# Kernel tuning notes

Hardware: AMD Instinct MI355X
Metric: run time of the kernel (lower is better)

The kernel has to match this reference:

```python
import jax, jax.numpy as jnp
import numpy as np

D_MODEL = 1024
NUM_HEADS = 16
HEAD_DIM = D_MODEL // NUM_HEADS
SCALE = HEAD_DIM ** -0.5
LN_EPS = 1e-5
Q_EPS = 1e-5


def bit_quant(W):
    # BitNet b1.58 ternary weight quantization with straight-through estimator.
    gamma = jnp.mean(jnp.abs(W))
    Wq = jnp.clip(jnp.round(W / (gamma + Q_EPS)), -1.0, 1.0) * gamma
    return W + jax.lax.stop_gradient(Wq - W)


def layer_norm(x, gamma, beta):
    mu = jnp.mean(x, axis=-1, keepdims=True)
    var = jnp.mean(jnp.square(x - mu), axis=-1, keepdims=True)
    return (x - mu) * jax.lax.rsqrt(var + LN_EPS) * gamma + beta


def setup_inputs() -> dict:
    key = jax.random.key(0)
    ks = jax.random.split(key, 8)
    B, T, T_ctx, C = 4, 1024, 2048, D_MODEL
    w_std = C ** -0.5
    return {
        "x": jax.random.normal(ks[0], (B, T, C), jnp.float32),
        "context": jax.random.normal(ks[1], (B, T_ctx, C), jnp.float32),
        "Wq": jax.random.normal(ks[2], (C, C), jnp.float32) * w_std,
        "bq": jnp.zeros((C,), jnp.float32),
        "Wk": jax.random.normal(ks[3], (C, C), jnp.float32) * w_std,
        "bk": jnp.zeros((C,), jnp.float32),
        "Wv": jax.random.normal(ks[4], (C, C), jnp.float32) * w_std,
        "bv": jnp.zeros((C,), jnp.float32),
        "Wo": jax.random.normal(ks[5], (C, C), jnp.float32) * w_std,
        "bo": jnp.zeros((C,), jnp.float32),
        "ln_gamma": jnp.ones((C,), jnp.float32),
        "ln_beta": jnp.zeros((C,), jnp.float32),
    }


def reference(x, context, Wq, bq, Wk, bk, Wv, bv, Wo, bo, ln_gamma, ln_beta):
    B, T, C = x.shape
    T_ctx = context.shape[1]
    residual = x
    xn = layer_norm(x, ln_gamma, ln_beta)
    # BitNet-quantized projections (torch Linear: y = x @ W.T + b)
    q = xn @ bit_quant(Wq).T + bq                      # [B,T,C]
    k = context @ bit_quant(Wk).T + bk                 # [B,T_ctx,C]
    v = context @ bit_quant(Wv).T + bv                 # [B,T_ctx,C]
    q = q.reshape(B, T, NUM_HEADS, HEAD_DIM)
    k = k.reshape(B, T_ctx, NUM_HEADS, HEAD_DIM)
    v = v.reshape(B, T_ctx, NUM_HEADS, HEAD_DIM)
    scores = jnp.einsum("bqhd,bkhd->bhqk", q, k) * SCALE   # [B,H,T,T_ctx]
    probs = jax.nn.softmax(scores, axis=-1)
    out = jnp.einsum("bhqk,bkhd->bqhd", probs, v).reshape(B, T, C)
    return residual + (out @ bit_quant(Wo).T + bo)
```

## Files before the change

### kernel.cpp

```cpp
#include <hip/hip_runtime.h>
#include <hip/hip_bf16.h>

typedef __attribute__((ext_vector_type(8))) short s8x;
typedef __attribute__((ext_vector_type(4))) float f4x;
typedef unsigned short u16;
typedef unsigned int u32;

#define T_ 1024
#define TC_ 2048
#define SCLOG2E 0.1803368801111243f

__device__ __forceinline__ u16 f2bf(float f) {
    u32 u = __float_as_uint(f);
    return (u16)((u + 0x7fffu + ((u >> 16) & 1u)) >> 16);
}

#if defined(__has_builtin)
#if __has_builtin(__builtin_amdgcn_cvt_pk_bf16_f32)
#define HAVE_PK 1
#endif
#endif

__device__ __forceinline__ u32 pack2bf(float a, float b) {
#ifdef HAVE_PK
    typedef __attribute__((ext_vector_type(2))) __bf16 bf2t;
    bf2t r = __builtin_amdgcn_cvt_pk_bf16_f32(a, b);
    u32 u;
    __builtin_memcpy(&u, &r, 4);
    return u;
#else
    return (u32)f2bf(a) | ((u32)f2bf(b) << 16);
#endif
}

__device__ __forceinline__ void gload16(const void* g, void* l) {
    __builtin_amdgcn_global_load_lds((const __attribute__((address_space(1))) u32*)g,
                                     (__attribute__((address_space(3))) u32*)l, 16, 0, 0);
}

__global__ __launch_bounds__(256) void absmean_k(const float* __restrict__ W0, const float* __restrict__ W1,
                                                 const float* __restrict__ W2, const float* __restrict__ W3,
                                                 float* __restrict__ gsum) {
    int wi = blockIdx.y;
    const float* W = (wi == 0) ? W0 : (wi == 1) ? W1 : (wi == 2) ? W2 : W3;
    const int n4 = (1024 * 1024) / 4;
    float s = 0.f;
    int stride = gridDim.x * blockDim.x;
    for (int i = blockIdx.x * blockDim.x + threadIdx.x; i < n4; i += stride) {
        float4 v = ((const float4*)W)[i];
        s += fabsf(v.x) + fabsf(v.y) + fabsf(v.z) + fabsf(v.w);
    }
#pragma unroll
    for (int off = 32; off; off >>= 1) s += __shfl_down(s, off, 64);
    __shared__ float ps[4];
    if ((threadIdx.x & 63) == 0) ps[threadIdx.x >> 6] = s;
    __syncthreads();
    if (threadIdx.x == 0) atomicAdd(gsum + wi, ps[0] + ps[1] + ps[2] + ps[3]);
}

__global__ __launch_bounds__(256) void prep_k(
        const float* __restrict__ x, const float* __restrict__ lng, const float* __restrict__ lnb,
        u16* __restrict__ xn,
        const float* __restrict__ ctx, u16* __restrict__ ctxb,
        const float* __restrict__ W0, const float* __restrict__ W1,
        const float* __restrict__ W2, const float* __restrict__ W3,
        u16* __restrict__ D0, u16* __restrict__ D1, u16* __restrict__ D2, u16* __restrict__ D3,
        const float* __restrict__ gsum) {
    __shared__ float ps[8];
    int bx = blockIdx.x, t = threadIdx.x;
    if (bx < 4096) {
        int row = bx;
        float4 xv = ((const float4*)(x + (long)row * 1024))[t];
        float s = xv.x + xv.y + xv.z + xv.w;
        float s2 = xv.x * xv.x + xv.y * xv.y + xv.z * xv.z + xv.w * xv.w;
#pragma unroll
        for (int off = 32; off; off >>= 1) { s += __shfl_down(s, off, 64); s2 += __shfl_down(s2, off, 64); }
        if ((t & 63) == 0) { ps[t >> 6] = s; ps[4 + (t >> 6)] = s2; }
        __syncthreads();
        float S = ps[0] + ps[1] + ps[2] + ps[3];
        float S2 = ps[4] + ps[5] + ps[6] + ps[7];
        float mu = S * (1.f / 1024.f);
        float var = S2 * (1.f / 1024.f) - mu * mu;
        float rstd = rsqrtf(var + 1e-5f);
        float4 gv = ((const float4*)lng)[t];
        float4 bv = ((const float4*)lnb)[t];
        uint2 o;
        o.x = pack2bf((xv.x - mu) * rstd * gv.x + bv.x, (xv.y - mu) * rstd * gv.y + bv.y);
        o.y = pack2bf((xv.z - mu) * rstd * gv.z + bv.z, (xv.w - mu) * rstd * gv.w + bv.w);
        ((uint2*)(xn + (long)row * 1024))[t] = o;
    } else if (bx < 12288) {
        int i = (bx - 4096) * 256 + t;
        float4 v = ((const float4*)ctx)[i];
        uint2 o = {pack2bf(v.x, v.y), pack2bf(v.z, v.w)};
        ((uint2*)ctxb)[i] = o;
    } else {
        int wi = (bx - 12288) >> 10;
        const float* W = (wi == 0) ? W0 : (wi == 1) ? W1 : (wi == 2) ? W2 : W3;
        u16* D = (wi == 0) ? D0 : (wi == 1) ? D1 : (wi == 2) ? D2 : D3;
        float inv = 1.0f / (gsum[wi] * (1.0f / 1048576.0f) + 1e-5f);
        int i = ((bx - 12288) & 1023) * 256 + t;
        float4 wv = ((const float4*)W)[i];
        uint2 o;
        o.x = pack2bf(fminf(1.f, fmaxf(-1.f, rintf(wv.x * inv))),
                      fminf(1.f, fmaxf(-1.f, rintf(wv.y * inv))));
        o.y = pack2bf(fminf(1.f, fmaxf(-1.f, rintf(wv.z * inv))),
                      fminf(1.f, fmaxf(-1.f, rintf(wv.w * inv))));
        ((uint2*)D)[i] = o;
    }
}

__global__ __launch_bounds__(256) void gemm_fused(
        const u16* __restrict__ xn, const u16* __restrict__ ctxb,
        const u16* __restrict__ wtq, const u16* __restrict__ wtk, const u16* __restrict__ wtv,
        const float* __restrict__ bq, const float* __restrict__ bk, const float* __restrict__ bv,
        const float* __restrict__ gsum,
        u16* __restrict__ qb, u16* __restrict__ kb, u16* __restrict__ vtb) {
    __shared__ __align__(16) char smem[32768];
    int tid = threadIdx.x;
    int w = tid >> 6, l = tid & 63, lq = l & 15, lh = l >> 4;
    int wm = (w >> 1) * 64, wn = (w & 1) * 64;
    int bx = blockIdx.x;
    int xcd = bx & 7;
    int prob, m0, n0, gidx;
    const u16 *A, *Wt;
    const float* bias;
    float sc;
    if (bx < 256) {
        int local = bx >> 3;
        prob = 0; A = xn; Wt = wtq; bias = bq; sc = SCLOG2E; gidx = 0;
        m0 = (xcd * 4 + (local & 3)) * 128;
        n0 = (local >> 2) * 128;
    } else {
        int b = bx - 256;
        int local3 = b >> 3;
        int kv = local3 & 1;
        int idx = local3 >> 1;
        prob = 1 + kv; A = ctxb;
        Wt = kv ? wtv : wtk; bias = kv ? bv : bk; sc = 1.0f; gidx = 1 + kv;
        m0 = (xcd * 8 + (idx & 7)) * 128;
        n0 = (idx >> 3) * 128;
    }
    char* AsB = smem;
    char* BsB = smem + 16384;
    f4x acc[4][4] = {};
    int rb = tid >> 3;
    int cg = (tid & 7) ^ (rb & 7);
    const u16* Ag = A + (long)m0 * 1024 + cg * 8;
    const u16* Bg = Wt + (long)n0 * 1024 + cg * 8;
    for (int k0 = 0; k0 < 1024; k0 += 64) {
        __syncthreads();
#pragma unroll
        for (int i = 0; i < 4; i++) {
            gload16(Ag + (long)(i * 32 + rb) * 1024 + k0, AsB + (i * 256 + tid) * 16);
            gload16(Bg + (long)(i * 32 + rb) * 1024 + k0, BsB + (i * 256 + tid) * 16);
        }
        __syncthreads();
#pragma unroll
        for (int s = 0; s < 2; s++) {
            int sl = (s * 4 + lh) ^ (lq & 7);
            s8x af[4], bfr[4];
#pragma unroll
            for (int i = 0; i < 4; i++) {
                af[i] = *(const s8x*)(AsB + (wm + i * 16 + lq) * 128 + sl * 16);
                bfr[i] = *(const s8x*)(BsB + (wn + i * 16 + lq) * 128 + sl * 16);
            }
#pragma unroll
            for (int i = 0; i < 4; i++)
#pragma unroll
                for (int j = 0; j < 4; j++)
                    acc[i][j] = __builtin_amdgcn_mfma_f32_16x16x32_bf16(af[i], bfr[j], acc[i][j], 0, 0, 0);
        }
    }
    float gamma = gsum[gidx] * (1.0f / 1048576.0f) * sc;
    if (prob < 2) {
        u16* outq = (prob == 0) ? qb : kb;
        int tshift = (prob == 0) ? 10 : 11;
        int tmask = (1 << tshift) - 1;
#pragma unroll
        for (int i = 0; i < 4; i++) {
            int gr = m0 + wm + i * 16 + lh * 4;
#pragma unroll
            for (int j = 0; j < 4; j++) {
                int gc = n0 + wn + j * 16 + lq;
                float bb = bias[gc] * sc;
                int h = gc >> 6, d = gc & 63;
#pragma unroll
                for (int r = 0; r < 4; r++) {
                    int row = gr + r;
                    int bidx = row >> tshift, tt = row & tmask;
                    outq[((((long)(bidx * 16 + h)) << tshift) + tt) * 64 + d] = f2bf(acc[i][j][r] * gamma + bb);
                }
            }
        }
    } else {
        __syncthreads();
        char* Ct = smem;
#pragma unroll
        for (int i = 0; i < 4; i++) {
            int tt = wm + i * 16 + lh * 4;
#pragma unroll
            for (int j = 0; j < 4; j++) {
                int c = wn + j * 16 + lq;
                float bb = bias[n0 + c];
                uint2 pk;
                pk.x = pack2bf(acc[i][j][0] * gamma + bb, acc[i][j][1] * gamma + bb);
                pk.y = pack2bf(acc[i][j][2] * gamma + bb, acc[i][j][3] * gamma + bb);
                int slot = (tt >> 3) ^ (c & 15);
                *(uint2*)(Ct + c * 256 + slot * 16 + (tt & 7) * 2) = pk;
            }
        }
        __syncthreads();
        int bb2 = m0 >> 11, t0 = m0 & 2047;
#pragma unroll
        for (int it = 0; it < 8; it++) {
            int e = it * 256 + tid;
            int c = e >> 4, ch = e & 15;
            int slot = ch ^ (c & 15);
            s8x v = *(const s8x*)(Ct + c * 256 + slot * 16);
            int gcg = n0 + c;
            int h = gcg >> 6, d = gcg & 63;
            *(s8x*)(vtb + ((long)((bb2 * 16 + h) * 64 + d)) * TC_ + t0 + ch * 8) = v;
        }
    }
}

__global__ __launch_bounds__(256) void gemm_o(const u16* __restrict__ A, const u16* __restrict__ Wt,
                                              const float* __restrict__ bias, const float* __restrict__ gsum,
                                              const float* __restrict__ residual, float* __restrict__ outr) {
    __shared__ __align__(16) char smem[24576];
    int tid = threadIdx.x;
    int w = tid >> 6, l = tid & 63, lq = l & 15, lh = l >> 4;
    int wm = (w >> 1) * 64, wn = (w & 1) * 32;
    int bx = blockIdx.x;
    int xcd = bx & 7, local = bx >> 3;
    int m0 = (xcd * 4 + (local & 3)) * 128;
    int n0 = (local >> 2) * 64;
    char* AsB = smem;
    char* BsB = smem + 16384;
    f4x acc[4][2] = {};
    int rb = tid >> 3;
    int cg = (tid & 7) ^ (rb & 7);
    const u16* Ag = A + (long)m0 * 1024 + cg * 8;
    const u16* Bg = Wt + (long)n0 * 1024 + cg * 8;
    for (int k0 = 0; k0 < 1024; k0 += 64) {
        __syncthreads();
#pragma unroll
        for (int i = 0; i < 4; i++)
            gload16(Ag + (long)(i * 32 + rb) * 1024 + k0, AsB + (i * 256 + tid) * 16);
#pragma unroll
        for (int i = 0; i < 2; i++)
            gload16(Bg + (long)(i * 32 + rb) * 1024 + k0, BsB + (i * 256 + tid) * 16);
        __syncthreads();
#pragma unroll
        for (int s = 0; s < 2; s++) {
            int sl = (s * 4 + lh) ^ (lq & 7);
            s8x af[4], bfr[2];
#pragma unroll
            for (int i = 0; i < 4; i++)
                af[i] = *(const s8x*)(AsB + (wm + i * 16 + lq) * 128 + sl * 16);
#pragma unroll
            for (int j = 0; j < 2; j++)
                bfr[j] = *(const s8x*)(BsB + (wn + j * 16 + lq) * 128 + sl * 16);
#pragma unroll
            for (int i = 0; i < 4; i++)
#pragma unroll
                for (int j = 0; j < 2; j++)
                    acc[i][j] = __builtin_amdgcn_mfma_f32_16x16x32_bf16(af[i], bfr[j], acc[i][j], 0, 0, 0);
        }
    }
    float gamma = gsum[3] * (1.0f / 1048576.0f);
#pragma unroll
    for (int i = 0; i < 4; i++) {
        int gr = m0 + wm + i * 16 + lh * 4;
#pragma unroll
        for (int j = 0; j < 2; j++) {
            int gc = n0 + wn + j * 16 + lq;
            float bb = bias[gc];
#pragma unroll
            for (int r = 0; r < 4; r++) {
                long idx = (long)(gr + r) * 1024 + gc;
                outr[idx] = residual[idx] + acc[i][j][r] * gamma + bb;
            }
        }
    }
}

__global__ __launch_bounds__(512) void attn_k(const u16* __restrict__ qh, const u16* __restrict__ kh,
                                              const u16* __restrict__ vth, u16* __restrict__ attn) {
    __shared__ __align__(16) char smem[51200];
    int tid = threadIdx.x, w = tid >> 6, l = tid & 63, lq = l & 15, lh = l >> 4;
    int bh = blockIdx.x, q0 = blockIdx.y * 128;
    const u16* qp = qh + ((long)bh * T_ + q0) * 64;
    const u16* kp = kh + (long)bh * TC_ * 64;
    const u16* vp = vth + (long)bh * 64 * TC_;
#pragma unroll
    for (int i = 0; i < 2; i++) {
        int cid = i * 512 + tid;
        int r = cid >> 3, c = (cid & 7) ^ (r & 7);
        gload16(qp + r * 64 + c * 8, smem + cid * 16);
    }
    __syncthreads();
    s8x qf0, qf1;
    {
        int qrow = w * 16 + lq;
        qf0 = *(const s8x*)(smem + qrow * 128 + ((lh) ^ (qrow & 7)) * 16);
        qf1 = *(const s8x*)(smem + qrow * 128 + ((4 + lh) ^ (qrow & 7)) * 16);
    }
    __syncthreads();
#define STAGE_KV(kt, buf)                                                      \
    {                                                                          \
        char* Kb = smem + (buf) * 16384;                                       \
        char* Vb = Kb + 8192;                                                  \
        int r = tid >> 3, c = (tid & 7) ^ (r & 7);                             \
        gload16(kp + ((kt) * 64 + r) * 64 + c * 8, Kb + tid * 16);             \
        gload16(vp + (long)r * TC_ + (kt) * 64 + c * 8, Vb + tid * 16);        \
    }
    STAGE_KV(0, 0);
    f4x oacc[4] = {};
    f4x lrun = {};
    float mrun = -1e30f;
    const s8x ones = {16256, 16256, 16256, 16256, 16256, 16256, 16256, 16256};
    char* Psb = smem + 32768 + w * 2304;
    for (int kt = 0; kt < TC_ / 64; kt++) {
        __syncthreads();
        if (kt + 1 < TC_ / 64) STAGE_KV(kt + 1, (kt + 1) & 1);
        char* Ksb = smem + (kt & 1) * 16384;
        char* Vsb = Ksb + 8192;
        f4x z[4];
#pragma unroll
        for (int ni = 0; ni < 4; ni++) {
            int kr = ni * 16 + lq;
            s8x a0 = *(const s8x*)(Ksb + kr * 128 + ((lh) ^ (kr & 7)) * 16);
            s8x a1 = *(const s8x*)(Ksb + kr * 128 + ((4 + lh) ^ (kr & 7)) * 16);
            f4x zz = {0.f, 0.f, 0.f, 0.f};
            zz = __builtin_amdgcn_mfma_f32_16x16x32_bf16(a0, qf0, zz, 0, 0, 0);
            zz = __builtin_amdgcn_mfma_f32_16x16x32_bf16(a1, qf1, zz, 0, 0, 0);
            z[ni] = zz;
        }
        float mx = fmaxf(fmaxf(fmaxf(z[0][0], z[0][1]), fmaxf(z[0][2], z[0][3])),
                         fmaxf(fmaxf(z[1][0], z[1][1]), fmaxf(z[1][2], z[1][3])));
        mx = fmaxf(mx, fmaxf(fmaxf(fmaxf(z[2][0], z[2][1]), fmaxf(z[2][2], z[2][3])),
                             fmaxf(fmaxf(z[3][0], z[3][1]), fmaxf(z[3][2], z[3][3]))));
#pragma unroll
        for (int s = 1; s <= 32; s <<= 1) mx = fmaxf(mx, __shfl_xor(mx, s));
        float mn = fmaxf(mrun, mx);
        float al = __builtin_amdgcn_exp2f(mrun - mn);
        mrun = mn;
#pragma unroll
        for (int ni = 0; ni < 4; ni++) {
            uint2 pk;
            pk.x = pack2bf(__builtin_amdgcn_exp2f(z[ni][0] - mn), __builtin_amdgcn_exp2f(z[ni][1] - mn));
            pk.y = pack2bf(__builtin_amdgcn_exp2f(z[ni][2] - mn), __builtin_amdgcn_exp2f(z[ni][3] - mn));
            *(uint2*)(Psb + lq * 144 + ni * 32 + lh * 8) = pk;
        }
        if (al != 1.0f) {
#pragma unroll
            for (int nd = 0; nd < 4; nd++)
#pragma unroll
                for (int r = 0; r < 4; r++) oacc[nd][r] *= al;
#pragma unroll
            for (int r = 0; r < 4; r++) lrun[r] *= al;
        }
        s8x vf0[4], vf1[4];
#pragma unroll
        for (int nd = 0; nd < 4; nd++) {
            int vr = nd * 16 + lq;
            vf0[nd] = *(const s8x*)(Vsb + vr * 128 + ((lh) ^ (vr & 7)) * 16);
            vf1[nd] = *(const s8x*)(Vsb + vr * 128 + ((4 + lh) ^ (vr & 7)) * 16);
        }
        s8x pf0 = *(const s8x*)(Psb + lq * 144 + lh * 16);
        s8x pf1 = *(const s8x*)(Psb + lq * 144 + 64 + lh * 16);
        f4x rs = {0.f, 0.f, 0.f, 0.f};
        rs = __builtin_amdgcn_mfma_f32_16x16x32_bf16(pf0, ones, rs, 0, 0, 0);
        rs = __builtin_amdgcn_mfma_f32_16x16x32_bf16(pf1, ones, rs, 0, 0, 0);
#pragma unroll
        for (int r = 0; r < 4; r++) lrun[r] += rs[r];
#pragma unroll
        for (int nd = 0; nd < 4; nd++) {
            oacc[nd] = __builtin_amdgcn_mfma_f32_16x16x32_bf16(pf0, vf0[nd], oacc[nd], 0, 0, 0);
            oacc[nd] = __builtin_amdgcn_mfma_f32_16x16x32_bf16(pf1, vf1[nd], oacc[nd], 0, 0, 0);
        }
    }
    int b = bh >> 4, h = bh & 15;
#pragma unroll
    for (int r = 0; r < 4; r++) {
        int q = q0 + w * 16 + lh * 4 + r;
        float rcp = 1.f / lrun[r];
#pragma unroll
        for (int nd = 0; nd < 4; nd++)
            attn[((long)(b * T_ + q)) * 1024 + h * 64 + nd * 16 + lq] = f2bf(oacc[nd][r] * rcp);
    }
}

extern "C" void kernel_launch(void* const* d_in, const int* in_sizes, int n_in,
                              void* d_out, int out_size, void* d_ws, size_t ws_size,
                              hipStream_t stream) {
    const float* x   = (const float*)d_in[0];
    const float* ctx = (const float*)d_in[1];
    const float* Wq  = (const float*)d_in[2];
    const float* bq  = (const float*)d_in[3];
    const float* Wk  = (const float*)d_in[4];
    const float* bk  = (const float*)d_in[5];
    const float* Wv  = (const float*)d_in[6];
    const float* bv  = (const float*)d_in[7];
    const float* Wo  = (const float*)d_in[8];
    const float* bo  = (const float*)d_in[9];
    const float* lng = (const float*)d_in[10];
    const float* lnb = (const float*)d_in[11];
    float* out = (float*)d_out;

    char* ws = (char*)d_ws;
    float* gsum = (float*)ws;
    size_t off = 256;
    u16* wtq  = (u16*)(ws + off); off += (size_t)1024 * 1024 * 2;
    u16* wtk  = (u16*)(ws + off); off += (size_t)1024 * 1024 * 2;
    u16* wtv  = (u16*)(ws + off); off += (size_t)1024 * 1024 * 2;
    u16* wto  = (u16*)(ws + off); off += (size_t)1024 * 1024 * 2;
    u16* ctxb = (u16*)(ws + off); off += (size_t)8192 * 1024 * 2;
    u16* xn   = (u16*)(ws + off); off += (size_t)4096 * 1024 * 2;
    u16* qb_  = (u16*)(ws + off); off += (size_t)4096 * 1024 * 2;
    u16* kb   = (u16*)(ws + off); off += (size_t)8192 * 1024 * 2;
    u16* vtb  = (u16*)(ws + off); off += (size_t)8192 * 1024 * 2;
    u16* attnb = xn;

    hipMemsetAsync(gsum, 0, 16, stream);
    absmean_k<<<dim3(128, 4), 256, 0, stream>>>(Wq, Wk, Wv, Wo, gsum);
    prep_k<<<16384, 256, 0, stream>>>(x, lng, lnb, xn, ctx, ctxb,
                                      Wq, Wk, Wv, Wo, wtq, wtk, wtv, wto, gsum);
    gemm_fused<<<1280, 256, 0, stream>>>(xn, ctxb, wtq, wtk, wtv, bq, bk, bv, gsum, qb_, kb, vtb);
    attn_k<<<dim3(64, 8), 512, 0, stream>>>(qb_, kb, vtb, attnb);
    gemm_o<<<512, 256, 0, stream>>>(attnb, wto, bo, gsum, x, out);
}
```

Baseline: 271.0 us.

## Split attention over key dimension with separate merge kernel

Splits the attention kernel's key/value loop into two halves run by separate blocks (grid z=2), writing unnormalized fp32 partial outputs plus running max and sum to workspace. A new merge kernel rescales and combines the two halves, then writes the bf16 attention output. This doubles the block count from 512 to 1024 so the GPU's compute units are better occupied. The cost is an extra kernel launch and roughly 32 MB of fp32 partial-output traffic.

New measurement: 282.6 us. 4.3% more time.

```diff
diff --git a/kernel.cpp b/kernel.cpp
--- a/kernel.cpp
+++ b/kernel.cpp
@@ -286,13 +286,15 @@
 }
 
 __global__ __launch_bounds__(512) void attn_k(const u16* __restrict__ qh, const u16* __restrict__ kh,
-                                              const u16* __restrict__ vth, u16* __restrict__ attn) {
+                                              const u16* __restrict__ vth,
+                                              float* __restrict__ Opart, float* __restrict__ Mpart,
+                                              float* __restrict__ Lpart) {
     __shared__ __align__(16) char smem[51200];
     int tid = threadIdx.x, w = tid >> 6, l = tid & 63, lq = l & 15, lh = l >> 4;
-    int bh = blockIdx.x, q0 = blockIdx.y * 128;
+    int bh = blockIdx.x, q0 = blockIdx.y * 128, half = blockIdx.z;
     const u16* qp = qh + ((long)bh * T_ + q0) * 64;
-    const u16* kp = kh + (long)bh * TC_ * 64;
-    const u16* vp = vth + (long)bh * 64 * TC_;
+    const u16* kp = kh + (long)bh * TC_ * 64 + half * 1024 * 64;
+    const u16* vp = vth + (long)bh * 64 * TC_ + half * 1024;
 #pragma unroll
     for (int i = 0; i < 2; i++) {
         int cid = i * 512 + tid;
@@ -321,9 +323,9 @@
     float mrun = -1e30f;
     const s8x ones = {16256, 16256, 16256, 16256, 16256, 16256, 16256, 16256};
     char* Psb = smem + 32768 + w * 2304;
-    for (int kt = 0; kt < TC_ / 64; kt++) {
-        __syncthreads();
-        if (kt + 1 < TC_ / 64) STAGE_KV(kt + 1, (kt + 1) & 1);
+    for (int kt = 0; kt < 16; kt++) {
+        __syncthreads();
+        if (kt + 1 < 16) STAGE_KV(kt + 1, (kt + 1) & 1);
         char* Ksb = smem + (kt & 1) * 16384;
         char* Vsb = Ksb + 8192;
         f4x z[4];
@@ -381,14 +383,46 @@
             oacc[nd] = __builtin_amdgcn_mfma_f32_16x16x32_bf16(pf1, vf1[nd], oacc[nd], 0, 0, 0);
         }
     }
+    int pidx = (bh * 8 + blockIdx.y) * 2 + half;
+    float* Op = Opart + (long)pidx * 8192;
+#pragma unroll
+    for (int r = 0; r < 4; r++) {
+        int ql = w * 16 + lh * 4 + r;
+#pragma unroll
+        for (int nd = 0; nd < 4; nd++)
+            Op[ql * 64 + nd * 16 + lq] = oacc[nd][r];
+        if (lq == 0) Lpart[(long)pidx * 128 + ql] = lrun[r];
+    }
+    if (l == 0) Mpart[pidx * 8 + w] = mrun;
+}
+
+__global__ __launch_bounds__(256) void merge_k(const float* __restrict__ Opart,
+                                               const float* __restrict__ Mpart,
+                                               const float* __restrict__ Lpart,
+                                               u16* __restrict__ attn) {
+    int pg = blockIdx.x;
+    int bh = pg >> 3, qt = pg & 7;
+    int t = threadIdx.x;
+    int q = t >> 1, dh = (t & 1) * 32;
+    int p0 = pg * 2, p1 = pg * 2 + 1;
+    float m0 = Mpart[p0 * 8 + (q >> 4)], m1 = Mpart[p1 * 8 + (q >> 4)];
+    float l0 = Lpart[(long)p0 * 128 + q], l1 = Lpart[(long)p1 * 128 + q];
+    float M = fmaxf(m0, m1);
+    float a0 = __builtin_amdgcn_exp2f(m0 - M);
+    float a1 = __builtin_amdgcn_exp2f(m1 - M);
+    float rinv = 1.f / (l0 * a0 + l1 * a1);
+    a0 *= rinv; a1 *= rinv;
+    const float4* O0 = (const float4*)(Opart + (long)p0 * 8192 + q * 64 + dh);
+    const float4* O1 = (const float4*)(Opart + (long)p1 * 8192 + q * 64 + dh);
     int b = bh >> 4, h = bh & 15;
-#pragma unroll
-    for (int r = 0; r < 4; r++) {
-        int q = q0 + w * 16 + lh * 4 + r;
-        float rcp = 1.f / lrun[r];
-#pragma unroll
-        for (int nd = 0; nd < 4; nd++)
-            attn[((long)(b * T_ + q)) * 1024 + h * 64 + nd * 16 + lq] = f2bf(oacc[nd][r] * rcp);
+    uint2* dst = (uint2*)(attn + ((long)(b * T_ + qt * 128 + q)) * 1024 + h * 64 + dh);
+#pragma unroll
+    for (int i = 0; i < 8; i++) {
+        float4 v0 = O0[i], v1 = O1[i];
+        uint2 o;
+        o.x = pack2bf(v0.x * a0 + v1.x * a1, v0.y * a0 + v1.y * a1);
+        o.y = pack2bf(v0.z * a0 + v1.z * a1, v0.w * a0 + v1.w * a1);
+        dst[i] = o;
     }
 }
 
@@ -421,6 +455,9 @@
     u16* qb_  = (u16*)(ws + off); off += (size_t)4096 * 1024 * 2;
     u16* kb   = (u16*)(ws + off); off += (size_t)8192 * 1024 * 2;
     u16* vtb  = (u16*)(ws + off); off += (size_t)8192 * 1024 * 2;
+    float* Opart = (float*)(ws + off); off += (size_t)1024 * 8192 * 4;
+    float* Mpart = (float*)(ws + off); off += (size_t)1024 * 8 * 4;
+    float* Lpart = (float*)(ws + off); off += (size_t)1024 * 128 * 4;
     u16* attnb = xn;
 
     hipMemsetAsync(gsum, 0, 16, stream);
@@ -428,6 +465,7 @@
     prep_k<<<16384, 256, 0, stream>>>(x, lng, lnb, xn, ctx, ctxb,
                                       Wq, Wk, Wv, Wo, wtq, wtk, wtv, wto, gsum);
     gemm_fused<<<1280, 256, 0, stream>>>(xn, ctxb, wtq, wtk, wtv, bq, bk, bv, gsum, qb_, kb, vtb);
-    attn_k<<<dim3(64, 8), 512, 0, stream>>>(qb_, kb, vtb, attnb);
+    attn_k<<<dim3(64, 8, 2), 512, 0, stream>>>(qb_, kb, vtb, Opart, Mpart, Lpart);
+    merge_k<<<512, 256, 0, stream>>>(Opart, Mpart, Lpart, attnb);
     gemm_o<<<512, 256, 0, stream>>>(attnb, wto, bo, gsum, x, out);
 }
```
